# Optimization experiments

Hardware: AMD Instinct MI355X
Metric: run time of the kernel (lower is better)

Reference implementation:

```python
import jax, jax.numpy as jnp
import numpy as np

SLOPE = 10.0  # surrogate gradient sigmoid slope

@jax.custom_vjp
def surrogate_spike(u):
    # forward: Heaviside step (u > 0)
    return (u > 0).astype(u.dtype)

def _spike_fwd(u):
    return surrogate_spike(u), u

def _spike_bwd(u, g):
    s = jax.nn.sigmoid(SLOPE * u)
    return (g * SLOPE * s * (1.0 - s),)

surrogate_spike.defvjp(_spike_fwd, _spike_bwd)

V_RESET = 0.0


def setup_inputs() -> dict:
    key = jax.random.key(0)
    T, B, N = 64, 64, 16384
    x_seq = jax.random.normal(key, (T, B, N), dtype=jnp.float32)
    return {
        "x_seq": x_seq,
        "v_th": jnp.asarray(1.0, dtype=jnp.float32),
        "tau": jnp.asarray(2.0, dtype=jnp.float32),
    }


def reference(x_seq, v_th, tau):
    # PmLIF membrane recurrence over T timesteps.
    # h_t = v_{t-1} + (1/tau) * (-(v_{t-1} - v_reset) + x_t)
    # s_t = Heaviside(h_t - v_th)   (surrogate grad in bwd)
    # v_t = h_t * (1 - s_t) + v_reset * s_t
    def step(v, x):
        h = v + (1.0 / tau) * (-(v - V_RESET) + x)
        s = surrogate_spike(h - v_th)
        v_new = h * (1.0 - s) + V_RESET * s
        return v_new, s

    v0 = jnp.zeros_like(x_seq[0])
    _, spikes = jax.lax.scan(step, v0, x_seq)
    return spikes  # [T, B, N]
```

## Files before the change

kernel.cpp:

```cpp
#include <hip/hip_runtime.h>


constexpr int T_STEPS = 64;

typedef float f32x4 __attribute__((ext_vector_type(4)));

struct StepOut { float v; float s; };

__device__ __forceinline__ StepOut pmlif_step(float xv, float v,
                                              float inv_tau, float v_th) {
    const float t = __fsub_rn(xv, v);
    const float h = __fadd_rn(v, __fmul_rn(inv_tau, t));
    const float u = __fsub_rn(h, v_th);
    const bool  b = u > 0.0f;
    StepOut r;
    r.s = b ? 1.0f : 0.0f;
    r.v = b ? 0.0f : h;
    return r;
}

__global__ __launch_bounds__(256) void pmlif_scan_kernel(
    const f32x4* __restrict__ x,
    f32x4* __restrict__ out,
    const float* __restrict__ v_th_p,
    const float* __restrict__ tau_p,
    int n4)
{
    const int idx = blockIdx.x * blockDim.x + threadIdx.x;
    if (idx >= n4) return;

    const float v_th    = *v_th_p;
    const float inv_tau = __fdiv_rn(1.0f, *tau_p);

    const f32x4* __restrict__ xp = x + idx;
    f32x4* __restrict__ op = out + idx;

    float v0 = 0.f, v1 = 0.f, v2 = 0.f, v3 = 0.f;

#pragma unroll 16
    for (int t = 0; t < T_STEPS; ++t) {
        const f32x4 xv = __builtin_nontemporal_load(&xp[(size_t)t * n4]);
        const StepOut r0 = pmlif_step(xv.x, v0, inv_tau, v_th);
        const StepOut r1 = pmlif_step(xv.y, v1, inv_tau, v_th);
        const StepOut r2 = pmlif_step(xv.z, v2, inv_tau, v_th);
        const StepOut r3 = pmlif_step(xv.w, v3, inv_tau, v_th);
        v0 = r0.v; v1 = r1.v; v2 = r2.v; v3 = r3.v;
        f32x4 s;
        s.x = r0.s; s.y = r1.s; s.z = r2.s; s.w = r3.s;
        __builtin_nontemporal_store(s, &op[(size_t)t * n4]);
    }
}

extern "C" void kernel_launch(void* const* d_in, const int* in_sizes, int n_in,
                              void* d_out, int out_size, void* d_ws, size_t ws_size,
                              hipStream_t stream) {
    const float* x    = (const float*)d_in[0];
    const float* v_th = (const float*)d_in[1];
    const float* tau  = (const float*)d_in[2];
    float* out = (float*)d_out;

    const int total = in_sizes[0];
    const int bn    = total / T_STEPS;
    const int n4    = bn / 4;

    const int block = 256;
    const int grid  = (n4 + block - 1) / block;

    pmlif_scan_kernel<<<grid, block, 0, stream>>>(
        (const f32x4*)x, (f32x4*)out, v_th, tau, n4);
}
```

Before: 117.1 us.

## Use float2 per thread with register prefetch ring of eight timesteps

Each thread now handles two neurons with float2 accesses instead of four with float4, which doubles the thread count for more parallelism. A ring of eight prefetched input vectors in registers keeps loads for the next timestep group in flight while the current group is computed and stored. Launch bounds now request higher occupancy. The risk is narrower memory transactions per instruction and extra register pressure from the prefetch buffer.

Measured after the change: 102.2 us. 12.7% less time.

```diff
diff --git a/kernel.cpp b/kernel.cpp
--- a/kernel.cpp
+++ b/kernel.cpp
@@ -2,8 +2,10 @@
 
 
 constexpr int T_STEPS = 64;
+constexpr int PF      = 8;
+constexpr int NGRP    = T_STEPS / PF;
 
-typedef float f32x4 __attribute__((ext_vector_type(4)));
+typedef float f32x2 __attribute__((ext_vector_type(2)));
 
 struct StepOut { float v; float s; };
 
@@ -19,35 +21,56 @@
     return r;
 }
 
-__global__ __launch_bounds__(256) void pmlif_scan_kernel(
-    const f32x4* __restrict__ x,
-    f32x4* __restrict__ out,
+__global__ __launch_bounds__(256, 8) void pmlif_scan_kernel(
+    const f32x2* __restrict__ x,
+    f32x2* __restrict__ out,
     const float* __restrict__ v_th_p,
     const float* __restrict__ tau_p,
-    int n4)
+    int n2)
 {
     const int idx = blockIdx.x * blockDim.x + threadIdx.x;
-    if (idx >= n4) return;
+    if (idx >= n2) return;
 
     const float v_th    = *v_th_p;
     const float inv_tau = __fdiv_rn(1.0f, *tau_p);
 
-    const f32x4* __restrict__ xp = x + idx;
-    f32x4* __restrict__ op = out + idx;
+    const f32x2* __restrict__ xp = x + idx;
+    f32x2* __restrict__ op = out + idx;
+    const size_t step = (size_t)n2;
 
-    float v0 = 0.f, v1 = 0.f, v2 = 0.f, v3 = 0.f;
+    f32x2 buf[PF];
+#pragma unroll
+    for (int k = 0; k < PF; ++k)
+        buf[k] = __builtin_nontemporal_load(&xp[(size_t)k * step]);
 
-#pragma unroll 16
-    for (int t = 0; t < T_STEPS; ++t) {
-        const f32x4 xv = __builtin_nontemporal_load(&xp[(size_t)t * n4]);
-        const StepOut r0 = pmlif_step(xv.x, v0, inv_tau, v_th);
-        const StepOut r1 = pmlif_step(xv.y, v1, inv_tau, v_th);
-        const StepOut r2 = pmlif_step(xv.z, v2, inv_tau, v_th);
-        const StepOut r3 = pmlif_step(xv.w, v3, inv_tau, v_th);
-        v0 = r0.v; v1 = r1.v; v2 = r2.v; v3 = r3.v;
-        f32x4 s;
-        s.x = r0.s; s.y = r1.s; s.z = r2.s; s.w = r3.s;
-        __builtin_nontemporal_store(s, &op[(size_t)t * n4]);
+    float v0 = 0.f, v1 = 0.f;
+
+    for (int g = 0; g < NGRP - 1; ++g) {
+        const f32x2* __restrict__ xg = xp + (size_t)(g + 1) * PF * step;
+        f32x2* __restrict__ og = op + (size_t)g * PF * step;
+#pragma unroll
+        for (int k = 0; k < PF; ++k) {
+            const f32x2 xv = buf[k];
+            buf[k] = __builtin_nontemporal_load(&xg[(size_t)k * step]);
+            const StepOut r0 = pmlif_step(xv.x, v0, inv_tau, v_th);
+            const StepOut r1 = pmlif_step(xv.y, v1, inv_tau, v_th);
+            v0 = r0.v; v1 = r1.v;
+            f32x2 s; s.x = r0.s; s.y = r1.s;
+            __builtin_nontemporal_store(s, &og[(size_t)k * step]);
+        }
+    }
+
+    {
+        f32x2* __restrict__ og = op + (size_t)(NGRP - 1) * PF * step;
+#pragma unroll
+        for (int k = 0; k < PF; ++k) {
+            const f32x2 xv = buf[k];
+            const StepOut r0 = pmlif_step(xv.x, v0, inv_tau, v_th);
+            const StepOut r1 = pmlif_step(xv.y, v1, inv_tau, v_th);
+            v0 = r0.v; v1 = r1.v;
+            f32x2 s; s.x = r0.s; s.y = r1.s;
+            __builtin_nontemporal_store(s, &og[(size_t)k * step]);
+        }
     }
 }
 
@@ -61,11 +84,11 @@
 
     const int total = in_sizes[0];
     const int bn    = total / T_STEPS;
-    const int n4    = bn / 4;
+    const int n2    = bn / 2;
 
     const int block = 256;
-    const int grid  = (n4 + block - 1) / block;
+    const int grid  = (n2 + block - 1) / block;
 
     pmlif_scan_kernel<<<grid, block, 0, stream>>>(
-        (const f32x4*)x, (f32x4*)out, v_th, tau, n4);
+        (const f32x2*)x, (f32x2*)out, v_th, tau, n2);
 }
```
